# Kernel tuning notes

Measured on AMD Instinct MI355X. Metric: run time of the kernel, lower is better.

Reference implementation:

```python
import jax, jax.numpy as jnp
import numpy as np

# Hard-coded model hyperparams (RuntimeParams)
B, L, H, NH, FF, DEPTH = 256, 256, 128, 8, 512, 4
PEAK, NCAT, CVOC, KMAX, NNUM, NDIM, TSLOT = 500000, 8, 50001, 8, 4, 32, 256
SCALE = (H // NH) ** -0.5


def _ln(x, g, b):
    m = x.mean(-1, keepdims=True)
    v = ((x - m) ** 2).mean(-1, keepdims=True)
    return (x - m) / jnp.sqrt(v + 1e-5) * g + b


def _block(x, mask, p):
    ln1_g, ln1_b, qw, qb, ow, ob, w1, b1, w2, b2, ln2_g, ln2_b = p
    b, n, c = x.shape
    src = _ln(x, ln1_g, ln1_b)
    qkv = (src @ qw + qb).reshape(b, n, 3, NH, c // NH).transpose(2, 0, 3, 1, 4)
    q, k, v = qkv[0], qkv[1], qkv[2]  # [b, nh, n, dh]
    dots = jnp.einsum('bhid,bhjd->bhij', q, k) * SCALE
    dots = jnp.where(mask[:, None, None, :], dots, -jnp.inf)
    attn = jax.nn.softmax(dots, axis=-1)
    out = jnp.einsum('bhij,bhjd->bhid', attn, v).transpose(0, 2, 1, 3).reshape(b, n, c)
    x = x + out @ ow + ob
    h = _ln(x, ln2_g, ln2_b)
    h = jax.nn.gelu(h @ w1 + b1, approximate=False) @ w2 + b2
    return x + h


def _encode(cat_vals, cat_lens, num_arr, cat_tables, num_W):
    # Vectorized form of the per-sample _encode_fields python loop:
    # per categorical field: mean of embeddings over the ragged value list
    # per numeric field: bias-free linear projection; then mean over all fields.
    emb = cat_tables[jnp.arange(NCAT)[None, :, None], cat_vals]  # [B,F,K,H]
    pos = (jnp.arange(KMAX)[None, None, :] < cat_lens[:, :, None]).astype(emb.dtype)
    fc = (emb * pos[..., None]).sum(2) / cat_lens[:, :, None].astype(emb.dtype)  # [B,F,H]
    fn = jnp.einsum('bfd,fdh->bfh', num_arr, num_W)  # [B,Fn,H]
    return (fc.sum(1) + fn.sum(1)) / (NCAT + NNUM)  # mean over all fields


def setup_inputs() -> dict:
    key = jax.random.key(0)
    ks = iter(jax.random.split(key, 40))
    nk = lambda: next(ks)
    d = {}
    d['item_seq'] = jax.random.randint(nk(), (B, L), 0, PEAK + 5)
    d['action_seq'] = jax.random.randint(nk(), (B, L), 0, 5)
    d['time_diff'] = jax.random.randint(nk(), (B, L), 0, TSLOT)
    seq_lens = jax.random.randint(nk(), (B,), L // 2, L + 1)
    d['mask'] = jnp.arange(L)[None, :] < seq_lens[:, None]
    for pre in ('u', 'i'):
        vals = jax.random.randint(nk(), (B, NCAT, KMAX), 1, CVOC)
        lens = jax.random.randint(nk(), (B, NCAT), 1, KMAX + 1)
        vals = jnp.where(jnp.arange(KMAX)[None, None, :] < lens[:, :, None], vals, 0)
        d[pre + '_cat_vals'] = vals
        d[pre + '_cat_lens'] = lens
        d[pre + '_num'] = jax.random.normal(nk(), (B, NNUM, NDIM), dtype=jnp.float32)
    s = 0.02
    d['item_table'] = (jax.random.normal(nk(), (PEAK + 5, H), dtype=jnp.float32) * s).at[0].set(0.0)
    d['act_table'] = jax.random.normal(nk(), (5, H), dtype=jnp.float32) * s
    d['time_table'] = jax.random.normal(nk(), (TSLOT, H), dtype=jnp.float32) * s
    d['cat_tables'] = (jax.random.normal(nk(), (NCAT, CVOC, H), dtype=jnp.float32) * s).at[:, 0, :].set(0.0)
    d['num_W'] = jax.random.normal(nk(), (NNUM, NDIM, H), dtype=jnp.float32) * s
    d['global_token'] = jax.random.normal(nk(), (1, 1, H), dtype=jnp.float32)
    d['ln1_g'] = jnp.ones((DEPTH, H)); d['ln1_b'] = jnp.zeros((DEPTH, H))
    d['qkv_w'] = jax.random.normal(nk(), (DEPTH, H, 3 * H), dtype=jnp.float32) * s
    d['qkv_b'] = jnp.zeros((DEPTH, 3 * H))
    d['out_w'] = jax.random.normal(nk(), (DEPTH, H, H), dtype=jnp.float32) * s
    d['out_b'] = jnp.zeros((DEPTH, H))
    d['mlp_w1'] = jax.random.normal(nk(), (DEPTH, H, FF), dtype=jnp.float32) * s
    d['mlp_b1'] = jnp.zeros((DEPTH, FF))
    d['mlp_w2'] = jax.random.normal(nk(), (DEPTH, FF, H), dtype=jnp.float32) * s
    d['mlp_b2'] = jnp.zeros((DEPTH, H))
    d['ln2_g'] = jnp.ones((DEPTH, H)); d['ln2_b'] = jnp.zeros((DEPTH, H))
    d['bott_w'] = jax.random.normal(nk(), (H, H), dtype=jnp.float32) * s
    d['bott_b'] = jnp.zeros((H,))
    d['cls_w'] = jax.random.normal(nk(), (H, 1), dtype=jnp.float32) * s
    d['cls_b'] = jnp.zeros((1,))
    return d


def reference(item_seq, action_seq, time_diff, mask, u_cat_vals, u_cat_lens, u_num,
              i_cat_vals, i_cat_lens, i_num, item_table, act_table, time_table,
              cat_tables, num_W, global_token, ln1_g, ln1_b, qkv_w, qkv_b,
              out_w, out_b, mlp_w1, mlp_b1, mlp_w2, mlp_b2, ln2_g, ln2_b,
              bott_w, bott_b, cls_w, cls_b):
    b = item_seq.shape[0]
    seq_feat = item_table[item_seq] + act_table[action_seq] + time_table[time_diff]  # [B,L,H]
    u = _encode(u_cat_vals, u_cat_lens, u_num, cat_tables, num_W)[:, None, :]
    i = _encode(i_cat_vals, i_cat_lens, i_num, cat_tables, num_W)[:, None, :]
    cls = jnp.broadcast_to(global_token, (b, 1, H))
    x = jnp.concatenate([cls, u, i, seq_feat], axis=1)  # [B, 3+L, H]
    fmask = jnp.concatenate([jnp.ones((b, 3), dtype=bool), mask], axis=1)
    for dd in range(DEPTH):
        p = (ln1_g[dd], ln1_b[dd], qkv_w[dd], qkv_b[dd], out_w[dd], out_b[dd],
             mlp_w1[dd], mlp_b1[dd], mlp_w2[dd], mlp_b2[dd], ln2_g[dd], ln2_b[dd])
        x = _block(x, fmask, p)
    latent = x[:, 0, :]
    logits = (jax.nn.relu(latent @ bott_w + bott_b) @ cls_w + cls_b)[:, 0]
    embed = latent / jnp.maximum(jnp.linalg.norm(latent, axis=-1, keepdims=True), 1e-12)
    return logits, embed
```

## Files before the change

### kernel.cpp

```cpp
#include <hip/hip_runtime.h>
#include <cstdio>

#define BATCH 256
#define SEQL 256
#define NPOS 259
#define TTOK (BATCH*NPOS)
#define HD 128
#define NHEAD 8
#define FF 512
#define DEPTH 4
#define CVOC 50001

typedef unsigned short u16;
typedef unsigned int u32;
typedef __bf16 bf16x8 __attribute__((ext_vector_type(8)));
typedef float f32x4 __attribute__((ext_vector_type(4)));
typedef float f32x16 __attribute__((ext_vector_type(16)));

typedef const __attribute__((address_space(1))) u32 gas_u32;
typedef __attribute__((address_space(3))) u32 las_u32;
#define GLOAD16(gptr, lptr) \
  __builtin_amdgcn_global_load_lds((gas_u32*)(gptr), (las_u32*)(lptr), 16, 0, 0)

#define QSCALE 0.36067376022224085f

__device__ __forceinline__ u16 f2bf(float f) {
  u32 i = __float_as_uint(f);
  u32 r = (i + 0x7FFFu + ((i >> 16) & 1u)) >> 16;
  return (u16)r;
}

__global__ void k_transpose_all(const float* __restrict__ qkv_w, const float* __restrict__ out_w,
                                const float* __restrict__ w1, const float* __restrict__ w2,
                                u16* __restrict__ wT) {
  int idx = blockIdx.x * 256 + threadIdx.x;
  const float* in; int K, N, local;
  if (idx < 196608)      { in = qkv_w; K = 128; N = 384; local = idx; }
  else if (idx < 262144) { in = out_w; K = 128; N = 128; local = idx - 196608; }
  else if (idx < 524288) { in = w1;    K = 128; N = 512; local = idx - 262144; }
  else if (idx < 786432) { in = w2;    K = 512; N = 128; local = idx - 524288; }
  else return;
  int k = local % K; int rem = local / K; int n = rem % N; int d = rem / N;
  wT[idx] = f2bf(in[(d * K + k) * N + n]);
}

__global__ __launch_bounds__(128)
void k_build(const int* __restrict__ item_seq, const int* __restrict__ act_seq,
             const int* __restrict__ tdiff,
             const int* __restrict__ ucv, const int* __restrict__ ucl, const float* __restrict__ unum,
             const int* __restrict__ icv, const int* __restrict__ icl, const float* __restrict__ inum,
             const float* __restrict__ item_t, const float* __restrict__ act_t,
             const float* __restrict__ time_t, const float* __restrict__ cat_t,
             const float* __restrict__ numW, const float* __restrict__ gtok,
             const float* __restrict__ g, const float* __restrict__ be,
             float* __restrict__ x, u16* __restrict__ src) {
  int pos = blockIdx.x, b = blockIdx.y, h = threadIdx.x;
  float v;
  if (pos == 0) {
    v = gtok[h];
  } else if (pos <= 2) {
    const int* cv = (pos == 1) ? ucv : icv;
    const int* cl = (pos == 1) ? ucl : icl;
    const float* nm = (pos == 1) ? unum : inum;
    float acc = 0.f;
    for (int f = 0; f < 8; ++f) {
      float s = 0.f;
      for (int k = 0; k < 8; ++k) {
        int idx = cv[(b * 8 + f) * 8 + k];
        s += cat_t[((size_t)f * CVOC + idx) * HD + h];
      }
      acc += s / (float)cl[b * 8 + f];
    }
    for (int f = 0; f < 4; ++f)
      for (int d = 0; d < 32; ++d)
        acc += nm[(b * 4 + f) * 32 + d] * numW[(f * 32 + d) * HD + h];
    v = acc * (1.f / 12.f);
  } else {
    int l = pos - 3;
    v = item_t[(size_t)item_seq[b * SEQL + l] * HD + h]
      + act_t[(size_t)act_seq[b * SEQL + l] * HD + h]
      + time_t[(size_t)tdiff[b * SEQL + l] * HD + h];
  }
  size_t t = (size_t)b * NPOS + pos;
  x[t * HD + h] = v;
  __shared__ float red[2][2];
  float s = v, s2 = v * v;
  #pragma unroll
  for (int o = 32; o; o >>= 1) { s += __shfl_xor(s, o); s2 += __shfl_xor(s2, o); }
  if ((h & 63) == 0) { red[h >> 6][0] = s; red[h >> 6][1] = s2; }
  __syncthreads();
  float S = red[0][0] + red[1][0], S2 = red[0][1] + red[1][1];
  float mean = S * (1.f / HD);
  float rstd = rsqrtf(S2 * (1.f / HD) - mean * mean + 1e-5f);
  src[t * HD + h] = f2bf((v - mean) * rstd * g[h] + be[h]);
}

template <int NCH, int ACT, bool QS>
__global__ __launch_bounds__(256)
void k_gemm_nres(const u16* __restrict__ X, const u16* __restrict__ WT,
                 const float* __restrict__ bias, u16* __restrict__ outp) {
  const int K = 128, N = NCH * 128;
  __shared__ __align__(16) u16 lA[4][64 * 32];
  __shared__ __align__(16) u16 lB[128 * 32];
  const int tid = threadIdx.x;
  const int wave = tid >> 6, lane = tid & 63;
  const int row0 = blockIdx.x * 64;
  const int wr = (wave >> 1) * 32, wc = (wave & 1) * 64;
  const int sr = lane >> 2;
  const int sc = ((lane & 3) ^ ((lane >> 3) & 3)) << 3;
  const int q = lane & 15;
  const int cg = lane >> 4;
  const int rdoff = ((cg ^ ((q >> 1) & 3)) << 3);
  #pragma unroll
  for (int kt = 0; kt < 4; ++kt)
    GLOAD16(X + (size_t)(row0 + wave * 16 + sr) * K + kt * 32 + sc, &lA[kt][wave * 512]);
  const u16* gB0 = WT + (size_t)(wave * 16 + sr) * K + sc;
  const u16* gB1 = WT + (size_t)(64 + wave * 16 + sr) * K + sc;
  u16* lB0 = &lB[wave * 512];
  u16* lB1 = &lB[2048 + wave * 512];
  for (int nc = 0; nc < NCH; ++nc) {
    const size_t nbase = (size_t)nc * 128 * K;
    f32x4 acc[2][4] = {};
    for (int k0 = 0; k0 < K; k0 += 32) {
      __syncthreads();
      GLOAD16(gB0 + nbase + k0, lB0);
      GLOAD16(gB1 + nbase + k0, lB1);
      __syncthreads();
      const int kt = k0 >> 5;
      bf16x8 af[2], bf[4];
      #pragma unroll
      for (int i = 0; i < 2; ++i)
        af[i] = *(const bf16x8*)&lA[kt][(wr + i * 16 + q) * 32 + rdoff];
      #pragma unroll
      for (int j = 0; j < 4; ++j)
        bf[j] = *(const bf16x8*)&lB[(wc + j * 16 + q) * 32 + rdoff];
      #pragma unroll
      for (int i = 0; i < 2; ++i)
        #pragma unroll
        for (int j = 0; j < 4; ++j)
          acc[i][j] = __builtin_amdgcn_mfma_f32_16x16x32_bf16(af[i], bf[j], acc[i][j], 0, 0, 0);
    }
    const int rg4 = cg * 4;
    const float scl = (QS && nc == 0) ? QSCALE : 1.f;
    #pragma unroll
    for (int i = 0; i < 2; ++i) {
      #pragma unroll
      for (int j = 0; j < 4; ++j) {
        int col = nc * 128 + wc + j * 16 + q;
        float bv = bias[col];
        #pragma unroll
        for (int jj = 0; jj < 4; ++jj) {
          int row = row0 + wr + i * 16 + rg4 + jj;
          float v = acc[i][j][jj] + bv;
          if (ACT == 1) v = 0.5f * v * (1.f + erff(v * 0.70710678118654752f));
          if (QS) v *= scl;
          outp[(size_t)row * N + col] = f2bf(v);
        }
      }
    }
  }
}

__global__ __launch_bounds__(256)
void k_gemm_ln(const u16* __restrict__ X, const u16* __restrict__ WT,
               const float* __restrict__ bias, float* __restrict__ xio,
               const float* __restrict__ g, const float* __restrict__ be,
               u16* __restrict__ srcout, int K) {
  __shared__ __align__(16) u16 lA[64 * 32];
  __shared__ __align__(16) u16 lB[128 * 32];
  __shared__ float part[64][2][2];
  const int tid = threadIdx.x;
  const int wave = tid >> 6, lane = tid & 63;
  const int row0 = blockIdx.x * 64;
  const int wr = (wave >> 1) * 32, wc = (wave & 1) * 64;
  const int whalf = wave & 1;
  const int sr = lane >> 2;
  const int sc = ((lane & 3) ^ ((lane >> 3) & 3)) << 3;
  const u16* gA = X + (size_t)(row0 + wave * 16 + sr) * K + sc;
  const u16* gB0 = WT + (size_t)(wave * 16 + sr) * K + sc;
  const u16* gB1 = WT + (size_t)(64 + wave * 16 + sr) * K + sc;
  u16* lA0 = &lA[wave * 512];
  u16* lB0 = &lB[wave * 512];
  u16* lB1 = &lB[2048 + wave * 512];
  const int q = lane & 15;
  const int cg = lane >> 4;
  const int rdoff = ((cg ^ ((q >> 1) & 3)) << 3);
  f32x4 acc[2][4] = {};
  for (int k0 = 0; k0 < K; k0 += 32) {
    __syncthreads();
    GLOAD16(gA + k0, lA0);
    GLOAD16(gB0 + k0, lB0);
    GLOAD16(gB1 + k0, lB1);
    __syncthreads();
    bf16x8 af[2], bf[4];
    #pragma unroll
    for (int i = 0; i < 2; ++i)
      af[i] = *(const bf16x8*)&lA[(wr + i * 16 + q) * 32 + rdoff];
    #pragma unroll
    for (int j = 0; j < 4; ++j)
      bf[j] = *(const bf16x8*)&lB[(wc + j * 16 + q) * 32 + rdoff];
    #pragma unroll
    for (int i = 0; i < 2; ++i)
      #pragma unroll
      for (int j = 0; j < 4; ++j)
        acc[i][j] = __builtin_amdgcn_mfma_f32_16x16x32_bf16(af[i], bf[j], acc[i][j], 0, 0, 0);
  }
  const int rg4 = cg * 4;
  float ps[2][4], ps2[2][4];
  #pragma unroll
  for (int i = 0; i < 2; ++i)
    #pragma unroll
    for (int jj = 0; jj < 4; ++jj) { ps[i][jj] = 0.f; ps2[i][jj] = 0.f; }
  #pragma unroll
  for (int i = 0; i < 2; ++i) {
    #pragma unroll
    for (int j = 0; j < 4; ++j) {
      int col = wc + j * 16 + q;
      float bv = bias[col];
      #pragma unroll
      for (int jj = 0; jj < 4; ++jj) {
        int row = row0 + wr + i * 16 + rg4 + jj;
        float xv = xio[(size_t)row * 128 + col] + acc[i][j][jj] + bv;
        acc[i][j][jj] = xv;
        ps[i][jj] += xv;
        ps2[i][jj] += xv * xv;
      }
    }
  }
  #pragma unroll
  for (int o = 1; o < 16; o <<= 1) {
    #pragma unroll
    for (int i = 0; i < 2; ++i)
      #pragma unroll
      for (int jj = 0; jj < 4; ++jj) {
        ps[i][jj]  += __shfl_xor(ps[i][jj], o);
        ps2[i][jj] += __shfl_xor(ps2[i][jj], o);
      }
  }
  if (q == 0) {
    #pragma unroll
    for (int i = 0; i < 2; ++i)
      #pragma unroll
      for (int jj = 0; jj < 4; ++jj) {
        int rl = wr + i * 16 + rg4 + jj;
        part[rl][whalf][0] = ps[i][jj];
        part[rl][whalf][1] = ps2[i][jj];
      }
  }
  __syncthreads();
  #pragma unroll
  for (int i = 0; i < 2; ++i) {
    #pragma unroll
    for (int jj = 0; jj < 4; ++jj) {
      int rl = wr + i * 16 + rg4 + jj;
      float S  = part[rl][0][0] + part[rl][1][0];
      float S2 = part[rl][0][1] + part[rl][1][1];
      float mean = S * (1.f / 128.f);
      float rstd = rsqrtf(S2 * (1.f / 128.f) - mean * mean + 1e-5f);
      int row = row0 + rl;
      #pragma unroll
      for (int j = 0; j < 4; ++j) {
        int col = wc + j * 16 + q;
        float xv = acc[i][j][jj];
        xio[(size_t)row * 128 + col] = xv;
        srcout[(size_t)row * 128 + col] = f2bf((xv - mean) * rstd * g[col] + be[col]);
      }
    }
  }
}

#define VSTR2 296
__global__ __launch_bounds__(576)
void k_attn(const u16* __restrict__ qkv, const int* __restrict__ mask,
            u16* __restrict__ out) {
  int b = blockIdx.x, h = blockIdx.y;
  __shared__ __align__(16) u16 Klin[9 * 512];
  __shared__ __align__(16) u16 Vt[16 * VSTR2];
  __shared__ int part[4];
  const int tid = threadIdx.x;
  if (tid < 256) {
    int mv = (mask[b * SEQL + tid] != 0) ? 1 : 0;
    #pragma unroll
    for (int o = 32; o; o >>= 1) mv += __shfl_xor(mv, o);
    if ((tid & 63) == 0) part[tid >> 6] = mv;
  }
  {
    int r = tid >> 1, h2 = tid & 1;
    uint4 val = make_uint4(0, 0, 0, 0);
    if (r < NPOS)
      val = *(const uint4*)&qkv[((size_t)(b * NPOS + r)) * 384 + h * 16 + 128 + h2 * 8];
    *(uint4*)&Klin[(r >> 5) * 512 + h2 * 256 + (r & 31) * 8] = val;
  }
  if (tid < 288) {
    int r = tid;
    u16 tmp[16];
    if (r < NPOS) {
      const u16* vp = &qkv[((size_t)(b * NPOS + r)) * 384 + h * 16 + 256];
      *(uint4*)&tmp[0] = *(const uint4*)&vp[0];
      *(uint4*)&tmp[8] = *(const uint4*)&vp[8];
    } else {
      #pragma unroll
      for (int d = 0; d < 16; ++d) tmp[d] = 0;
    }
    #pragma unroll
    for (int d = 0; d < 16; ++d) Vt[d * VSTR2 + r] = tmp[d];
  }
  __syncthreads();
  const int nvalid = part[0] + part[1] + part[2] + part[3] + 3;
  const int ktiles = (nvalid + 31) >> 5;
  const int wave = tid >> 6, lane = tid & 63;
  const int q5 = lane & 31, hi = lane >> 5;
  const f32x16 zf = {};
  const int qt = wave;
  int qrow = qt * 32 + q5;
  int qr = (qrow < NPOS) ? qrow : (NPOS - 1);
  bf16x8 qf = *(const bf16x8*)&qkv[((size_t)(b * NPOS + qr)) * 384 + h * 16 + hi * 8];
  float m = -1e30f, l = 0.f;
  f32x16 acc = {};
  for (int kt = 0; kt < ktiles; ++kt) {
    bf16x8 kf = *(const bf16x8*)&Klin[kt * 512 + lane * 8];
    __builtin_amdgcn_s_setprio(1);
    f32x16 s4 = __builtin_amdgcn_mfma_f32_32x32x16_bf16(kf, qf, zf, 0, 0, 0);
    __builtin_amdgcn_s_setprio(0);
    float p[16];
    float tmax = -1e30f;
    #pragma unroll
    for (int r = 0; r < 16; ++r) {
      int kr = kt * 32 + (r & 3) + 8 * (r >> 2) + 4 * hi;
      float v = (kr < nvalid) ? s4[r] : -1e30f;
      p[r] = v;
      tmax = fmaxf(tmax, v);
    }
    tmax = fmaxf(tmax, __shfl_xor(tmax, 32));
    bool defer = __all(tmax <= m + 8.f);
    float mnew = defer ? m : fmaxf(m, tmax);
    float fac = defer ? 1.f : exp2f(m - mnew);
    float tsum = 0.f;
    #pragma unroll
    for (int r = 0; r < 16; ++r) { p[r] = exp2f(p[r] - mnew); tsum += p[r]; }
    tsum += __shfl_xor(tsum, 32);
    l = l * fac + tsum;
    m = mnew;
    if (!defer) {
      #pragma unroll
      for (int r = 0; r < 8; ++r) acc[r] *= fac;
    }
    u32 w[8], xw[8];
    #pragma unroll
    for (int i = 0; i < 8; ++i)
      asm("v_cvt_pk_bf16_f32 %0, %1, %2" : "=v"(w[i]) : "v"(p[2 * i]), "v"(p[2 * i + 1]));
    #pragma unroll
    for (int i = 0; i < 8; ++i) xw[i] = (u32)__shfl_xor((int)w[i], 32);
    union { u32 u[4]; bf16x8 v; } f1, f2;
    if (hi) {
      f1.u[0] = xw[2]; f1.u[1] = xw[3]; f1.u[2] = w[2]; f1.u[3] = w[3];
      f2.u[0] = xw[6]; f2.u[1] = xw[7]; f2.u[2] = w[6]; f2.u[3] = w[7];
    } else {
      f1.u[0] = w[0]; f1.u[1] = w[1]; f1.u[2] = xw[0]; f1.u[3] = xw[1];
      f2.u[0] = w[4]; f2.u[1] = w[5]; f2.u[2] = xw[4]; f2.u[3] = xw[5];
    }
    bf16x8 vf0 = {}, vf1 = {};
    if (q5 < 16) {
      vf0 = *(const bf16x8*)&Vt[q5 * VSTR2 + kt * 32 + hi * 8];
      vf1 = *(const bf16x8*)&Vt[q5 * VSTR2 + kt * 32 + 16 + hi * 8];
    }
    __builtin_amdgcn_s_setprio(1);
    acc = __builtin_amdgcn_mfma_f32_32x32x16_bf16(vf0, f1.v, acc, 0, 0, 0);
    acc = __builtin_amdgcn_mfma_f32_32x32x16_bf16(vf1, f2.v, acc, 0, 0, 0);
    __builtin_amdgcn_s_setprio(0);
  }
  if (qrow < NPOS) {
    float linv = 1.f / l;
    u16* op = &out[((size_t)(b * NPOS + qrow)) * HD + h * 16];
    u32 w0 = (u32)f2bf(acc[0] * linv) | ((u32)f2bf(acc[1] * linv) << 16);
    u32 w1 = (u32)f2bf(acc[2] * linv) | ((u32)f2bf(acc[3] * linv) << 16);
    u32 w2 = (u32)f2bf(acc[4] * linv) | ((u32)f2bf(acc[5] * linv) << 16);
    u32 w3 = (u32)f2bf(acc[6] * linv) | ((u32)f2bf(acc[7] * linv) << 16);
    *(uint2*)&op[4 * hi] = make_uint2(w0, w1);
    *(uint2*)&op[8 + 4 * hi] = make_uint2(w2, w3);
  }
}

__global__ __launch_bounds__(128)
void k_head(const float* __restrict__ x, const float* __restrict__ bw,
            const float* __restrict__ bb, const float* __restrict__ cw,
            const float* __restrict__ cb, float* __restrict__ dout) {
  int b = blockIdx.x, n = threadIdx.x;
  __shared__ float lat[HD];
  __shared__ float redp[2], redss[2];
  float lv = x[((size_t)b * NPOS) * HD + n];
  lat[n] = lv;
  __syncthreads();
  float t = 0.f;
  for (int k = 0; k < HD; ++k) t += lat[k] * bw[k * HD + n];
  t += bb[n];
  t = fmaxf(t, 0.f);
  float p = t * cw[n];
  float ss = lv * lv;
  #pragma unroll
  for (int o = 32; o; o >>= 1) { p += __shfl_xor(p, o); ss += __shfl_xor(ss, o); }
  if ((n & 63) == 0) { redp[n >> 6] = p; redss[n >> 6] = ss; }
  __syncthreads();
  float psum = redp[0] + redp[1];
  float ssum = redss[0] + redss[1];
  if (n == 0) dout[b] = psum + cb[0];
  float nrm = fmaxf(sqrtf(ssum), 1e-12f);
  dout[256 + (size_t)b * HD + n] = lv / nrm;
}

extern "C" void kernel_launch(void* const* d_in, const int* in_sizes, int n_in,
                              void* d_out, int out_size, void* d_ws, size_t ws_size,
                              hipStream_t stream) {
  const int* item_seq = (const int*)d_in[0];
  const int* action_seq = (const int*)d_in[1];
  const int* time_diff = (const int*)d_in[2];
  const int* mask = (const int*)d_in[3];
  const int* u_cv = (const int*)d_in[4];
  const int* u_cl = (const int*)d_in[5];
  const float* u_num = (const float*)d_in[6];
  const int* i_cv = (const int*)d_in[7];
  const int* i_cl = (const int*)d_in[8];
  const float* i_num = (const float*)d_in[9];
  const float* item_t = (const float*)d_in[10];
  const float* act_t = (const float*)d_in[11];
  const float* time_t = (const float*)d_in[12];
  const float* cat_t = (const float*)d_in[13];
  const float* num_W = (const float*)d_in[14];
  const float* gtok = (const float*)d_in[15];
  const float* ln1_g = (const float*)d_in[16];
  const float* ln1_b = (const float*)d_in[17];
  const float* qkv_w = (const float*)d_in[18];
  const float* qkv_b = (const float*)d_in[19];
  const float* out_w = (const float*)d_in[20];
  const float* out_b = (const float*)d_in[21];
  const float* w1 = (const float*)d_in[22];
  const float* b1 = (const float*)d_in[23];
  const float* w2 = (const float*)d_in[24];
  const float* b2 = (const float*)d_in[25];
  const float* ln2_g = (const float*)d_in[26];
  const float* ln2_b = (const float*)d_in[27];
  const float* bott_w = (const float*)d_in[28];
  const float* bott_b = (const float*)d_in[29];
  const float* cls_w = (const float*)d_in[30];
  const float* cls_b = (const float*)d_in[31];

  const size_t off_x   = 0;
  const size_t off_src = 33947648;
  const size_t off_big = 50921472;
  const size_t off_wT  = 118816768;
  const size_t need    = 120389632;
  if (ws_size < need) {
    fprintf(stderr, "kernel_launch: ws_size %zu < needed %zu\n", ws_size, need);
    return;
  }
  char* ws = (char*)d_ws;
  float* x   = (float*)(ws + off_x);
  u16* src   = (u16*)(ws + off_src);
  u16* big   = (u16*)(ws + off_big);
  u16* wT    = (u16*)(ws + off_wT);
  u16* qkvT  = wT;
  u16* outT  = wT + 196608;
  u16* w1T   = wT + 262144;
  u16* w2T   = wT + 524288;

  k_transpose_all<<<3072, 256, 0, stream>>>(qkv_w, out_w, w1, w2, wT);

  k_build<<<dim3(NPOS, BATCH), 128, 0, stream>>>(
      item_seq, action_seq, time_diff, u_cv, u_cl, u_num, i_cv, i_cl, i_num,
      item_t, act_t, time_t, cat_t, num_W, gtok, ln1_g, ln1_b, x, src);

  const int rt = TTOK / 64;
  for (int dd = 0; dd < DEPTH; ++dd) {
    k_gemm_nres<3, 0, true><<<rt, 256, 0, stream>>>(
        src, qkvT + dd * 49152, qkv_b + dd * 384, big);
    k_attn<<<dim3(BATCH, NHEAD), 576, 0, stream>>>(big, mask, src);
    k_gemm_ln<<<rt, 256, 0, stream>>>(
        src, outT + dd * 16384, out_b + dd * HD, x,
        ln2_g + dd * HD, ln2_b + dd * HD, src, 128);
    k_gemm_nres<4, 1, false><<<rt, 256, 0, stream>>>(
        src, w1T + dd * 65536, b1 + dd * FF, big);
    const float* ng = (dd < 3) ? (ln1_g + (dd + 1) * HD) : (ln1_g + dd * HD);
    const float* nb = (dd < 3) ? (ln1_b + (dd + 1) * HD) : (ln1_b + dd * HD);
    k_gemm_ln<<<rt, 256, 0, stream>>>(
        big, w2T + dd * 65536, b2 + dd * HD, x, ng, nb, src, 512);
  }

  k_head<<<BATCH, 128, 0, stream>>>(x, bott_w, bott_b, cls_w, cls_b, (float*)d_out);
}
```

Baseline: 722.2 us.

## Store residual stream in bf16 and widen V transpose loads across threads

The residual activations x are now stored as bf16 instead of fp32 across the build, the fused GEMM+LayerNorm, and the head kernels. This halves the residual read/write traffic in every layer and shrinks the workspace. It also spreads the V-transpose staging in attention over twice as many threads with 16-byte loads each. The risk is extra rounding error that accumulates in the residual over the four layers.

```diff
diff --git a/kernel.cpp b/kernel.cpp
--- a/kernel.cpp
+++ b/kernel.cpp
@@ -28,6 +28,9 @@
   u32 i = __float_as_uint(f);
   u32 r = (i + 0x7FFFu + ((i >> 16) & 1u)) >> 16;
   return (u16)r;
+}
+__device__ __forceinline__ float bf2f(u16 u) {
+  return __uint_as_float(((u32)u) << 16);
 }
 
 __global__ void k_transpose_all(const float* __restrict__ qkv_w, const float* __restrict__ out_w,
@@ -53,7 +56,7 @@
              const float* __restrict__ time_t, const float* __restrict__ cat_t,
              const float* __restrict__ numW, const float* __restrict__ gtok,
              const float* __restrict__ g, const float* __restrict__ be,
-             float* __restrict__ x, u16* __restrict__ src) {
+             u16* __restrict__ x, u16* __restrict__ src) {
   int pos = blockIdx.x, b = blockIdx.y, h = threadIdx.x;
   float v;
   if (pos == 0) {
@@ -82,7 +85,7 @@
       + time_t[(size_t)tdiff[b * SEQL + l] * HD + h];
   }
   size_t t = (size_t)b * NPOS + pos;
-  x[t * HD + h] = v;
+  x[t * HD + h] = f2bf(v);
   __shared__ float red[2][2];
   float s = v, s2 = v * v;
   #pragma unroll
@@ -163,7 +166,7 @@
 
 __global__ __launch_bounds__(256)
 void k_gemm_ln(const u16* __restrict__ X, const u16* __restrict__ WT,
-               const float* __restrict__ bias, float* __restrict__ xio,
+               const float* __restrict__ bias, u16* __restrict__ xio,
                const float* __restrict__ g, const float* __restrict__ be,
                u16* __restrict__ srcout, int K) {
   __shared__ __align__(16) u16 lA[64 * 32];
@@ -220,7 +223,7 @@
       #pragma unroll
       for (int jj = 0; jj < 4; ++jj) {
         int row = row0 + wr + i * 16 + rg4 + jj;
-        float xv = xio[(size_t)row * 128 + col] + acc[i][j][jj] + bv;
+        float xv = bf2f(xio[(size_t)row * 128 + col]) + acc[i][j][jj] + bv;
         acc[i][j][jj] = xv;
         ps[i][jj] += xv;
         ps2[i][jj] += xv * xv;
@@ -262,7 +265,7 @@
       for (int j = 0; j < 4; ++j) {
         int col = wc + j * 16 + q;
         float xv = acc[i][j][jj];
-        xio[(size_t)row * 128 + col] = xv;
+        xio[(size_t)row * 128 + col] = f2bf(xv);
         srcout[(size_t)row * 128 + col] = f2bf((xv - mean) * rstd * g[col] + be[col]);
       }
     }
@@ -291,19 +294,19 @@
       val = *(const uint4*)&qkv[((size_t)(b * NPOS + r)) * 384 + h * 16 + 128 + h2 * 8];
     *(uint4*)&Klin[(r >> 5) * 512 + h2 * 256 + (r & 31) * 8] = val;
   }
-  if (tid < 288) {
-    int r = tid;
-    u16 tmp[16];
-    if (r < NPOS) {
-      const u16* vp = &qkv[((size_t)(b * NPOS + r)) * 384 + h * 16 + 256];
-      *(uint4*)&tmp[0] = *(const uint4*)&vp[0];
-      *(uint4*)&tmp[8] = *(const uint4*)&vp[8];
-    } else {
-      #pragma unroll
-      for (int d = 0; d < 16; ++d) tmp[d] = 0;
-    }
-    #pragma unroll
-    for (int d = 0; d < 16; ++d) Vt[d * VSTR2 + r] = tmp[d];
+  {
+    int r = tid >> 1, h2 = tid & 1;
+    if (r < 288) {
+      u16 tmp[8];
+      if (r < NPOS) {
+        *(uint4*)tmp = *(const uint4*)&qkv[((size_t)(b * NPOS + r)) * 384 + h * 16 + 256 + h2 * 8];
+      } else {
+        #pragma unroll
+        for (int d = 0; d < 8; ++d) tmp[d] = 0;
+      }
+      #pragma unroll
+      for (int d = 0; d < 8; ++d) Vt[(h2 * 8 + d) * VSTR2 + r] = tmp[d];
+    }
   }
   __syncthreads();
   const int nvalid = part[0] + part[1] + part[2] + part[3] + 3;
@@ -382,13 +385,13 @@
 }
 
 __global__ __launch_bounds__(128)
-void k_head(const float* __restrict__ x, const float* __restrict__ bw,
+void k_head(const u16* __restrict__ x, const float* __restrict__ bw,
             const float* __restrict__ bb, const float* __restrict__ cw,
             const float* __restrict__ cb, float* __restrict__ dout) {
   int b = blockIdx.x, n = threadIdx.x;
   __shared__ float lat[HD];
   __shared__ float redp[2], redss[2];
-  float lv = x[((size_t)b * NPOS) * HD + n];
+  float lv = bf2f(x[((size_t)b * NPOS) * HD + n]);
   lat[n] = lv;
   __syncthreads();
   float t = 0.f;
@@ -445,16 +448,16 @@
   const float* cls_b = (const float*)d_in[31];
 
   const size_t off_x   = 0;
-  const size_t off_src = 33947648;
-  const size_t off_big = 50921472;
-  const size_t off_wT  = 118816768;
-  const size_t need    = 120389632;
+  const size_t off_src = 16973824;
+  const size_t off_big = 33947648;
+  const size_t off_wT  = 101842944;
+  const size_t need    = 103415808;
   if (ws_size < need) {
     fprintf(stderr, "kernel_launch: ws_size %zu < needed %zu\n", ws_size, need);
     return;
   }
   char* ws = (char*)d_ws;
-  float* x   = (float*)(ws + off_x);
+  u16* x     = (u16*)(ws + off_x);
   u16* src   = (u16*)(ws + off_src);
   u16* big   = (u16*)(ws + off_big);
   u16* wT    = (u16*)(ws + off_wT);
```

Result: faster. 704.8 us (-2.4%).
